# Kernel tuning notes

Measured on AMD Instinct MI355X. Metric: run time of the kernel, lower is better.

Reference implementation:

```python
import jax, jax.numpy as jnp
import numpy as np

NUM_HEADS = 12
HEAD_DIM = 64
EPS = 1e-6


def rms_norm(x, w):
    # normalize over last dim (head_dim)
    norm = jax.lax.rsqrt(jnp.mean(x * x, axis=-1, keepdims=True) + EPS)
    return x * norm * w


def apply_rotary_emb(x, cos, sin):
    x1, x2 = jnp.split(x, 2, axis=-1)
    return jnp.concatenate([x1 * cos - x2 * sin, x2 * cos + x1 * sin], axis=-1)


def setup_inputs() -> dict:
    key = jax.random.key(0)
    ks = jax.random.split(key, 6)
    B, N, C = 4, 2048, 768
    return {
        "x": jax.random.normal(ks[0], (B, N, C), dtype=jnp.float32),
        "cos": jax.random.uniform(ks[1], (1, 1, N, HEAD_DIM // 2), dtype=jnp.float32),
        "sin": jax.random.uniform(ks[2], (1, 1, N, HEAD_DIM // 2), dtype=jnp.float32),
        "qkv_w": jax.random.normal(ks[3], (3 * C, C), dtype=jnp.float32) * (C ** -0.5),
        "q_norm_w": jnp.ones((HEAD_DIM,), dtype=jnp.float32),
        "k_norm_w": jnp.ones((HEAD_DIM,), dtype=jnp.float32),
        "proj_w": jax.random.normal(ks[4], (C, C), dtype=jnp.float32) * (C ** -0.5),
        "proj_b": jnp.zeros((C,), dtype=jnp.float32),
    }


def reference(x, cos, sin, qkv_w, q_norm_w, k_norm_w, proj_w, proj_b):
    B, N, C = x.shape
    H, D = NUM_HEADS, HEAD_DIM
    scale = D ** -0.5
    # qkv projection: [B,N,3C] -> [3,B,H,N,D]
    qkv = jnp.einsum('bnc,oc->bno', x, qkv_w)
    qkv = qkv.reshape(B, N, 3, H, D).transpose(2, 0, 3, 1, 4)
    q, k, v = qkv[0], qkv[1], qkv[2]
    q = rms_norm(q, q_norm_w)
    k = rms_norm(k, k_norm_w)
    q = apply_rotary_emb(q, cos, sin)
    k = apply_rotary_emb(k, cos, sin)
    attn = jnp.einsum('bhqd,bhkd->bhqk', q, k) * scale
    attn = jax.nn.softmax(attn, axis=-1)
    out = jnp.einsum('bhqk,bhkd->bhqd', attn, v)
    out = out.transpose(0, 2, 1, 3).reshape(B, N, C)
    out = jnp.einsum('bnc,oc->bno', out, proj_w) + proj_b
    return out
```

## Files before the change

### kernel.cpp

```cpp
#include <hip/hip_runtime.h>
#include <hip/hip_bf16.h>

#define BB 4
#define NN 2048
#define CC 768
#define HH 12
#define DD 64

typedef __bf16 bf16;
typedef __attribute__((ext_vector_type(8))) __bf16 bf16x8;
typedef __attribute__((ext_vector_type(4))) __bf16 bf16x4;
typedef __attribute__((ext_vector_type(4))) float f32x4;

#define SZ_X    (BB * NN * CC)
#define SZ_QKVW (3 * CC * CC)
#define SZ_PW   (CC * CC)
#define SZ_QKV  ((size_t)BB * NN * 3 * CC)

#define OFF_X    0
#define OFF_QW   (OFF_X + SZ_X)
#define OFF_PW   (OFF_QW + SZ_QKVW)
#define OFF_QKV  (OFF_PW + SZ_PW)

__device__ __forceinline__ void async16(const bf16* g, bf16* l) {
    __builtin_amdgcn_global_load_lds(
        (const __attribute__((address_space(1))) unsigned int*)g,
        (__attribute__((address_space(3))) unsigned int*)l, 16, 0, 0);
}

__device__ __forceinline__ void cast8(const float* __restrict__ src,
                                      bf16* __restrict__ dst, int i) {
    f32x4 a = ((const f32x4*)src)[2 * i];
    f32x4 b = ((const f32x4*)src)[2 * i + 1];
    bf16x8 o;
#pragma unroll
    for (int j = 0; j < 4; ++j) { o[j] = (bf16)a[j]; o[j + 4] = (bf16)b[j]; }
    ((bf16x8*)dst)[i] = o;
}

__global__ __launch_bounds__(256) void convert3(
    const float* __restrict__ x, const float* __restrict__ qkvw,
    const float* __restrict__ pw, bf16* __restrict__ ws) {
    const int t = blockIdx.x * 256 + threadIdx.x;
    const int S = gridDim.x * 256;
    for (int i = t; i < SZ_X / 8;    i += S) cast8(x,    ws + OFF_X,  i);
    for (int i = t; i < SZ_QKVW / 8; i += S) cast8(qkvw, ws + OFF_QW, i);
    for (int i = t; i < SZ_PW / 8;   i += S) cast8(pw,   ws + OFF_PW, i);
}

__global__ __launch_bounds__(256) void gemm_qkv(
    const bf16* __restrict__ A, const bf16* __restrict__ W,
    bf16* __restrict__ C, bf16* __restrict__ Vt,
    const float* __restrict__ cosb, const float* __restrict__ sinb,
    const float* __restrict__ qw, const float* __restrict__ kw) {
    __shared__ __align__(16) bf16 As[128 * 64];
    __shared__ __align__(16) bf16 Bs[128 * 64];
    const int tid  = threadIdx.x;
    const int wave = tid >> 6;
    const int lane = tid & 63;
    const int quad = lane >> 4;
    const int l16  = lane & 15;
    const int m0 = blockIdx.y * 128;
    const int n0 = blockIdx.x * 128;
    const int wm = (wave >> 1) * 64;
    const int wn = (wave & 1) * 64;
    const int srow = lane >> 3;
    const int swz  = (lane & 7) ^ srow;
    const int K = CC;
    const int Nn = 3 * CC;

    f32x4 acc[4][4];
#pragma unroll
    for (int i = 0; i < 4; ++i)
#pragma unroll
        for (int j = 0; j < 4; ++j) acc[i][j] = (f32x4){0.f, 0.f, 0.f, 0.f};

    for (int k0 = 0; k0 < K; k0 += 64) {
#pragma unroll
        for (int i = 0; i < 4; ++i) {
            int row = i * 32 + wave * 8 + srow;
            async16(A + (size_t)(m0 + row) * CC + k0 + swz * 8,
                    &As[(i * 32 + wave * 8) * 64]);
            async16(W + (size_t)(n0 + row) * K + k0 + swz * 8,
                    &Bs[(i * 32 + wave * 8) * 64]);
        }
        __syncthreads();
#pragma unroll
        for (int kk = 0; kk < 2; ++kk) {
            const int slot = ((kk * 4 + quad) ^ (l16 & 7)) * 8;
            bf16x8 af[4], bf[4];
#pragma unroll
            for (int mt = 0; mt < 4; ++mt)
                af[mt] = *(const bf16x8*)(&As[(wm + mt * 16 + l16) * 64 + slot]);
#pragma unroll
            for (int nt = 0; nt < 4; ++nt)
                bf[nt] = *(const bf16x8*)(&Bs[(wn + nt * 16 + l16) * 64 + slot]);
#pragma unroll
            for (int mt = 0; mt < 4; ++mt)
#pragma unroll
                for (int nt = 0; nt < 4; ++nt)
                    acc[mt][nt] = __builtin_amdgcn_mfma_f32_16x16x32_bf16(
                        af[mt], bf[nt], acc[mt][nt], 0, 0, 0);
        }
        __syncthreads();
    }

    const int colblk = n0 + wn;
    const int sector = colblk / CC;
    if (sector == 2) {
        const int head = (colblk >> 6) - 24;
        const int btok = m0 + wm;
        const int bh   = (btok >> 11) * HH + head;
        const int nloc = btok & (NN - 1);
#pragma unroll
        for (int nt = 0; nt < 4; ++nt) {
            const int d = nt * 16 + l16;
            bf16* dst = Vt + ((size_t)bh * DD + d) * NN + nloc + quad * 4;
#pragma unroll
            for (int mt = 0; mt < 4; ++mt) {
                bf16x4 pk;
#pragma unroll
                for (int r = 0; r < 4; ++r) pk[r] = (bf16)acc[mt][nt][r];
                *(bf16x4*)(dst + mt * 16) = pk;
            }
        }
    } else {
        const float* wp = (sector == 0) ? qw : kw;
        const float qs = (sector == 0) ? 0.18033688f : 1.0f;
        float wv[4];
#pragma unroll
        for (int nt = 0; nt < 4; ++nt) wv[nt] = wp[nt * 16 + l16];
#pragma unroll
        for (int mt = 0; mt < 4; ++mt)
#pragma unroll
            for (int r = 0; r < 4; ++r) {
                const int row = m0 + wm + mt * 16 + quad * 4 + r;
                const int n   = row & (NN - 1);
                float v[4];
#pragma unroll
                for (int nt = 0; nt < 4; ++nt) v[nt] = acc[mt][nt][r];
                float ss = v[0] * v[0] + v[1] * v[1] + v[2] * v[2] + v[3] * v[3];
                ss += __shfl_xor(ss, 1, 64);
                ss += __shfl_xor(ss, 2, 64);
                ss += __shfl_xor(ss, 4, 64);
                ss += __shfl_xor(ss, 8, 64);
                const float rn = rsqrtf(ss * (1.0f / 64.0f) + 1e-6f);
#pragma unroll
                for (int nt = 0; nt < 4; ++nt) v[nt] *= rn * wv[nt];
                const float c0 = cosb[n * 32 + l16];
                const float c1 = cosb[n * 32 + 16 + l16];
                const float s0 = sinb[n * 32 + l16];
                const float s1 = sinb[n * 32 + 16 + l16];
                float y[4];
                y[0] = v[0] * c0 - v[2] * s0;
                y[1] = v[1] * c1 - v[3] * s1;
                y[2] = v[2] * c0 + v[0] * s0;
                y[3] = v[3] * c1 + v[1] * s1;
#pragma unroll
                for (int nt = 0; nt < 4; ++nt) {
                    int col = colblk + nt * 16 + l16;
                    C[(size_t)row * Nn + col] = (bf16)(y[nt] * qs);
                }
            }
    }
}

__global__ __launch_bounds__(256) void gemm_proj(
    const bf16* __restrict__ A, const bf16* __restrict__ W,
    const float* __restrict__ bias, float* __restrict__ C) {
    __shared__ __align__(16) bf16 As[128 * 64];
    __shared__ __align__(16) bf16 Bs[64 * 64];
    const int tid  = threadIdx.x;
    const int wave = tid >> 6;
    const int lane = tid & 63;
    const int quad = lane >> 4;
    const int l16  = lane & 15;
    const int m0 = blockIdx.y * 128;
    const int n0 = blockIdx.x * 64;
    const int wm = (wave >> 1) * 64;
    const int wn = (wave & 1) * 32;
    const int srow = lane >> 3;
    const int swz  = (lane & 7) ^ srow;
    const int lda = 3 * CC;
    const int K = CC;

    f32x4 acc[4][2];
#pragma unroll
    for (int i = 0; i < 4; ++i)
#pragma unroll
        for (int j = 0; j < 2; ++j) acc[i][j] = (f32x4){0.f, 0.f, 0.f, 0.f};

    for (int k0 = 0; k0 < K; k0 += 64) {
#pragma unroll
        for (int i = 0; i < 4; ++i) {
            int row = i * 32 + wave * 8 + srow;
            async16(A + (size_t)(m0 + row) * lda + k0 + swz * 8,
                    &As[(i * 32 + wave * 8) * 64]);
        }
#pragma unroll
        for (int i = 0; i < 2; ++i) {
            int row = i * 32 + wave * 8 + srow;
            async16(W + (size_t)(n0 + row) * K + k0 + swz * 8,
                    &Bs[(i * 32 + wave * 8) * 64]);
        }
        __syncthreads();
#pragma unroll
        for (int kk = 0; kk < 2; ++kk) {
            const int slot = ((kk * 4 + quad) ^ (l16 & 7)) * 8;
            bf16x8 af[4], bf[2];
#pragma unroll
            for (int mt = 0; mt < 4; ++mt)
                af[mt] = *(const bf16x8*)(&As[(wm + mt * 16 + l16) * 64 + slot]);
#pragma unroll
            for (int nt = 0; nt < 2; ++nt)
                bf[nt] = *(const bf16x8*)(&Bs[(wn + nt * 16 + l16) * 64 + slot]);
#pragma unroll
            for (int mt = 0; mt < 4; ++mt)
#pragma unroll
                for (int nt = 0; nt < 2; ++nt)
                    acc[mt][nt] = __builtin_amdgcn_mfma_f32_16x16x32_bf16(
                        af[mt], bf[nt], acc[mt][nt], 0, 0, 0);
        }
        __syncthreads();
    }
#pragma unroll
    for (int mt = 0; mt < 4; ++mt)
#pragma unroll
        for (int nt = 0; nt < 2; ++nt)
#pragma unroll
            for (int r = 0; r < 4; ++r) {
                int row = m0 + wm + mt * 16 + quad * 4 + r;
                int col = n0 + wn + nt * 16 + l16;
                C[(size_t)row * CC + col] = acc[mt][nt][r] + bias[col];
            }
}

__global__ __launch_bounds__(256) void flash_attn(
    const bf16* __restrict__ qkv, const bf16* __restrict__ Vt,
    bf16* __restrict__ Oqkv) {
    __shared__ __align__(16) bf16 Ks[64 * 64];
    __shared__ __align__(16) bf16 Vs[64 * 64];
    __shared__ __align__(16) bf16 Ps[4][32 * 72];
    const int tid  = threadIdx.x;
    const int wave = tid >> 6;
    const int lane = tid & 63;
    const int quad = lane >> 4;
    const int l16  = lane & 15;
    const int r7   = l16 & 7;
    const int bh = blockIdx.x;
    const int qt = blockIdx.y;
    const int b = bh / HH, h = bh % HH;
    const size_t rs = 3 * CC;
    const bf16* Qb  = qkv + (size_t)b * NN * rs + h * DD;
    const bf16* Kb  = Qb + CC;
    const bf16* Vtb = Vt + (size_t)bh * DD * NN;

    bf16x8 qf[2][2];
#pragma unroll
    for (int f = 0; f < 2; ++f) {
        const int qrow = qt * 128 + wave * 32 + f * 16 + l16;
#pragma unroll
        for (int hf = 0; hf < 2; ++hf)
            qf[f][hf] = *(const bf16x8*)(Qb + (size_t)qrow * rs + hf * 32 + quad * 8);
    }

    f32x4 accO[2][4];
#pragma unroll
    for (int f = 0; f < 2; ++f)
#pragma unroll
        for (int i = 0; i < 4; ++i) accO[f][i] = (f32x4){0.f, 0.f, 0.f, 0.f};
    float lsum[2] = {0.f, 0.f};

    const int srow = lane >> 3;
    const int swz  = (lane & 7) ^ srow;

    for (int kt = 0; kt < NN / 64; ++kt) {
#pragma unroll
        for (int i = 0; i < 2; ++i) {
            int row = i * 32 + wave * 8 + srow;
            async16(Kb + (size_t)(kt * 64 + row) * rs + swz * 8,
                    &Ks[(i * 32 + wave * 8) * 64]);
            async16(Vtb + (size_t)row * NN + kt * 64 + swz * 8,
                    &Vs[(i * 32 + wave * 8) * 64]);
        }
        __syncthreads();

        f32x4 s[2][4];
#pragma unroll
        for (int nt = 0; nt < 4; ++nt) {
            const int row = nt * 16 + l16;
            bf16x8 kf0 = *(const bf16x8*)(&Ks[row * 64 + (quad ^ r7) * 8]);
            bf16x8 kf1 = *(const bf16x8*)(&Ks[row * 64 + ((quad + 4) ^ r7) * 8]);
#pragma unroll
            for (int f = 0; f < 2; ++f) {
                f32x4 z = (f32x4){0.f, 0.f, 0.f, 0.f};
                z = __builtin_amdgcn_mfma_f32_16x16x32_bf16(kf0, qf[f][0], z, 0, 0, 0);
                s[f][nt] = __builtin_amdgcn_mfma_f32_16x16x32_bf16(kf1, qf[f][1], z, 0, 0, 0);
            }
        }

#pragma unroll
        for (int f = 0; f < 2; ++f)
#pragma unroll
            for (int nt = 0; nt < 4; ++nt) {
                bf16x4 pk;
#pragma unroll
                for (int r = 0; r < 4; ++r) {
                    float pv = __builtin_amdgcn_exp2f(s[f][nt][r]);
                    lsum[f] += pv;
                    pk[r] = (bf16)pv;
                }
                *(bf16x4*)(&Ps[wave][(f * 16 + l16) * 72 + nt * 16 + quad * 4]) = pk;
            }
        __asm__ volatile("s_waitcnt lgkmcnt(0)" ::: "memory");

        bf16x8 pf0[2], pf1[2];
#pragma unroll
        for (int f = 0; f < 2; ++f) {
            pf0[f] = *(const bf16x8*)(&Ps[wave][(f * 16 + l16) * 72 + quad * 8]);
            pf1[f] = *(const bf16x8*)(&Ps[wave][(f * 16 + l16) * 72 + 32 + quad * 8]);
        }
#pragma unroll
        for (int nt = 0; nt < 4; ++nt) {
            const int rowd = nt * 16 + l16;
            bf16x8 vf0 = *(const bf16x8*)(&Vs[rowd * 64 + (quad ^ r7) * 8]);
            bf16x8 vf1 = *(const bf16x8*)(&Vs[rowd * 64 + ((quad + 4) ^ r7) * 8]);
#pragma unroll
            for (int f = 0; f < 2; ++f) {
                accO[f][nt] = __builtin_amdgcn_mfma_f32_16x16x32_bf16(pf0[f], vf0, accO[f][nt], 0, 0, 0);
                accO[f][nt] = __builtin_amdgcn_mfma_f32_16x16x32_bf16(pf1[f], vf1, accO[f][nt], 0, 0, 0);
            }
        }
        __syncthreads();
    }

#pragma unroll
    for (int f = 0; f < 2; ++f) {
        lsum[f] += __shfl_xor(lsum[f], 16, 64);
        lsum[f] += __shfl_xor(lsum[f], 32, 64);
    }

#pragma unroll
    for (int f = 0; f < 2; ++f)
#pragma unroll
        for (int r = 0; r < 4; ++r) {
            float inv = 1.0f / __shfl(lsum[f], quad * 4 + r, 64);
            int n = qt * 128 + wave * 32 + f * 16 + quad * 4 + r;
#pragma unroll
            for (int nt = 0; nt < 4; ++nt) {
                int col = h * DD + nt * 16 + l16;
                Oqkv[(size_t)(b * NN + n) * rs + 2 * CC + col] = (bf16)(accO[f][nt][r] * inv);
            }
        }
}

extern "C" void kernel_launch(void* const* d_in, const int* in_sizes, int n_in,
                              void* d_out, int out_size, void* d_ws, size_t ws_size,
                              hipStream_t stream) {
    const float* x     = (const float*)d_in[0];
    const float* cosb  = (const float*)d_in[1];
    const float* sinb  = (const float*)d_in[2];
    const float* qkv_w = (const float*)d_in[3];
    const float* qnw   = (const float*)d_in[4];
    const float* knw   = (const float*)d_in[5];
    const float* pw    = (const float*)d_in[6];
    const float* pb    = (const float*)d_in[7];
    float* out = (float*)d_out;

    bf16* ws  = (bf16*)d_ws;
    bf16* xb  = ws + OFF_X;
    bf16* qwb = ws + OFF_QW;
    bf16* pwb = ws + OFF_PW;
    bf16* qkv = ws + OFF_QKV;
    bf16* vt  = (bf16*)d_out;

    const int M = BB * NN;

    convert3<<<1024, 256, 0, stream>>>(x, qkv_w, pw, ws);

    dim3 g1(3 * CC / 128, M / 128);
    gemm_qkv<<<g1, 256, 0, stream>>>(xb, qwb, qkv, vt, cosb, sinb, qnw, knw);

    dim3 g4(BB * HH, NN / 128);
    flash_attn<<<g4, 256, 0, stream>>>(qkv, vt, qkv);

    dim3 g5(CC / 64, M / 128);
    gemm_proj<<<g5, 256, 0, stream>>>(qkv + 2 * CC, pwb, pb, out);
}
```

Measured before the change: 231.4 us.

## Split flash attention work across 8 waves with 16 query rows each

The attention kernel now launches 512 threads per block, and each of 8 waves handles 16 query rows instead of 4 waves handling 32. K/V tile loads are spread over more threads, with one async load per thread per tile, and per-wave registers and P scratch shrink. This aims to raise parallelism and latency hiding. The cost is that each K/V fragment read from LDS is reused by only one query fragment, which doubles LDS reads per MFMA, and the block barriers now span more waves.

```diff
diff --git a/kernel.cpp b/kernel.cpp
--- a/kernel.cpp
+++ b/kernel.cpp
@@ -235,12 +235,12 @@
             }
 }
 
-__global__ __launch_bounds__(256) void flash_attn(
+__global__ __launch_bounds__(512) void flash_attn(
     const bf16* __restrict__ qkv, const bf16* __restrict__ Vt,
     bf16* __restrict__ Oqkv) {
     __shared__ __align__(16) bf16 Ks[64 * 64];
     __shared__ __align__(16) bf16 Vs[64 * 64];
-    __shared__ __align__(16) bf16 Ps[4][32 * 72];
+    __shared__ __align__(16) bf16 Ps[8][16 * 72];
     const int tid  = threadIdx.x;
     const int wave = tid >> 6;
     const int lane = tid & 63;
@@ -255,103 +255,80 @@
     const bf16* Kb  = Qb + CC;
     const bf16* Vtb = Vt + (size_t)bh * DD * NN;
 
-    bf16x8 qf[2][2];
-#pragma unroll
-    for (int f = 0; f < 2; ++f) {
-        const int qrow = qt * 128 + wave * 32 + f * 16 + l16;
+    bf16x8 qf[2];
+    {
+        const int qrow = qt * 128 + wave * 16 + l16;
 #pragma unroll
         for (int hf = 0; hf < 2; ++hf)
-            qf[f][hf] = *(const bf16x8*)(Qb + (size_t)qrow * rs + hf * 32 + quad * 8);
-    }
-
-    f32x4 accO[2][4];
-#pragma unroll
-    for (int f = 0; f < 2; ++f)
-#pragma unroll
-        for (int i = 0; i < 4; ++i) accO[f][i] = (f32x4){0.f, 0.f, 0.f, 0.f};
-    float lsum[2] = {0.f, 0.f};
+            qf[hf] = *(const bf16x8*)(Qb + (size_t)qrow * rs + hf * 32 + quad * 8);
+    }
+
+    f32x4 accO[4];
+#pragma unroll
+    for (int i = 0; i < 4; ++i) accO[i] = (f32x4){0.f, 0.f, 0.f, 0.f};
+    float lsum = 0.f;
 
     const int srow = lane >> 3;
     const int swz  = (lane & 7) ^ srow;
+    const int strow = wave * 8 + srow;
 
     for (int kt = 0; kt < NN / 64; ++kt) {
-#pragma unroll
-        for (int i = 0; i < 2; ++i) {
-            int row = i * 32 + wave * 8 + srow;
-            async16(Kb + (size_t)(kt * 64 + row) * rs + swz * 8,
-                    &Ks[(i * 32 + wave * 8) * 64]);
-            async16(Vtb + (size_t)row * NN + kt * 64 + swz * 8,
-                    &Vs[(i * 32 + wave * 8) * 64]);
-        }
-        __syncthreads();
-
-        f32x4 s[2][4];
+        async16(Kb + (size_t)(kt * 64 + strow) * rs + swz * 8,
+                &Ks[(wave * 8) * 64]);
+        async16(Vtb + (size_t)strow * NN + kt * 64 + swz * 8,
+                &Vs[(wave * 8) * 64]);
+        __syncthreads();
+
+        f32x4 s[4];
 #pragma unroll
         for (int nt = 0; nt < 4; ++nt) {
             const int row = nt * 16 + l16;
             bf16x8 kf0 = *(const bf16x8*)(&Ks[row * 64 + (quad ^ r7) * 8]);
             bf16x8 kf1 = *(const bf16x8*)(&Ks[row * 64 + ((quad + 4) ^ r7) * 8]);
-#pragma unroll
-            for (int f = 0; f < 2; ++f) {
-                f32x4 z = (f32x4){0.f, 0.f, 0.f, 0.f};
-                z = __builtin_amdgcn_mfma_f32_16x16x32_bf16(kf0, qf[f][0], z, 0, 0, 0);
-                s[f][nt] = __builtin_amdgcn_mfma_f32_16x16x32_bf16(kf1, qf[f][1], z, 0, 0, 0);
+            f32x4 z = (f32x4){0.f, 0.f, 0.f, 0.f};
+            z = __builtin_amdgcn_mfma_f32_16x16x32_bf16(kf0, qf[0], z, 0, 0, 0);
+            s[nt] = __builtin_amdgcn_mfma_f32_16x16x32_bf16(kf1, qf[1], z, 0, 0, 0);
+        }
+
+#pragma unroll
+        for (int nt = 0; nt < 4; ++nt) {
+            bf16x4 pk;
+#pragma unroll
+            for (int r = 0; r < 4; ++r) {
+                float pv = __builtin_amdgcn_exp2f(s[nt][r]);
+                lsum += pv;
+                pk[r] = (bf16)pv;
             }
-        }
-
-#pragma unroll
-        for (int f = 0; f < 2; ++f)
-#pragma unroll
-            for (int nt = 0; nt < 4; ++nt) {
-                bf16x4 pk;
-#pragma unroll
-                for (int r = 0; r < 4; ++r) {
-                    float pv = __builtin_amdgcn_exp2f(s[f][nt][r]);
-                    lsum[f] += pv;
-                    pk[r] = (bf16)pv;
-                }
-                *(bf16x4*)(&Ps[wave][(f * 16 + l16) * 72 + nt * 16 + quad * 4]) = pk;
-            }
+            *(bf16x4*)(&Ps[wave][l16 * 72 + nt * 16 + quad * 4]) = pk;
+        }
         __asm__ volatile("s_waitcnt lgkmcnt(0)" ::: "memory");
 
-        bf16x8 pf0[2], pf1[2];
-#pragma unroll
-        for (int f = 0; f < 2; ++f) {
-            pf0[f] = *(const bf16x8*)(&Ps[wave][(f * 16 + l16) * 72 + quad * 8]);
-            pf1[f] = *(const bf16x8*)(&Ps[wave][(f * 16 + l16) * 72 + 32 + quad * 8]);
-        }
+        bf16x8 pf0 = *(const bf16x8*)(&Ps[wave][l16 * 72 + quad * 8]);
+        bf16x8 pf1 = *(const bf16x8*)(&Ps[wave][l16 * 72 + 32 + quad * 8]);
 #pragma unroll
         for (int nt = 0; nt < 4; ++nt) {
             const int rowd = nt * 16 + l16;
             bf16x8 vf0 = *(const bf16x8*)(&Vs[rowd * 64 + (quad ^ r7) * 8]);
             bf16x8 vf1 = *(const bf16x8*)(&Vs[rowd * 64 + ((quad + 4) ^ r7) * 8]);
-#pragma unroll
-            for (int f = 0; f < 2; ++f) {
-                accO[f][nt] = __builtin_amdgcn_mfma_f32_16x16x32_bf16(pf0[f], vf0, accO[f][nt], 0, 0, 0);
-                accO[f][nt] = __builtin_amdgcn_mfma_f32_16x16x32_bf16(pf1[f], vf1, accO[f][nt], 0, 0, 0);
-            }
-        }
-        __syncthreads();
-    }
-
-#pragma unroll
-    for (int f = 0; f < 2; ++f) {
-        lsum[f] += __shfl_xor(lsum[f], 16, 64);
-        lsum[f] += __shfl_xor(lsum[f], 32, 64);
-    }
-
-#pragma unroll
-    for (int f = 0; f < 2; ++f)
-#pragma unroll
-        for (int r = 0; r < 4; ++r) {
-            float inv = 1.0f / __shfl(lsum[f], quad * 4 + r, 64);
-            int n = qt * 128 + wave * 32 + f * 16 + quad * 4 + r;
-#pragma unroll
-            for (int nt = 0; nt < 4; ++nt) {
-                int col = h * DD + nt * 16 + l16;
-                Oqkv[(size_t)(b * NN + n) * rs + 2 * CC + col] = (bf16)(accO[f][nt][r] * inv);
-            }
-        }
+            accO[nt] = __builtin_amdgcn_mfma_f32_16x16x32_bf16(pf0, vf0, accO[nt], 0, 0, 0);
+            accO[nt] = __builtin_amdgcn_mfma_f32_16x16x32_bf16(pf1, vf1, accO[nt], 0, 0, 0);
+        }
+        __syncthreads();
+    }
+
+    lsum += __shfl_xor(lsum, 16, 64);
+    lsum += __shfl_xor(lsum, 32, 64);
+
+#pragma unroll
+    for (int r = 0; r < 4; ++r) {
+        float inv = 1.0f / __shfl(lsum, quad * 4 + r, 64);
+        int n = qt * 128 + wave * 16 + quad * 4 + r;
+#pragma unroll
+        for (int nt = 0; nt < 4; ++nt) {
+            int col = h * DD + nt * 16 + l16;
+            Oqkv[(size_t)(b * NN + n) * rs + 2 * CC + col] = (bf16)(accO[nt][r] * inv);
+        }
+    }
 }
 
 extern "C" void kernel_launch(void* const* d_in, const int* in_sizes, int n_in,
@@ -382,7 +359,7 @@
     gemm_qkv<<<g1, 256, 0, stream>>>(xb, qwb, qkv, vt, cosb, sinb, qnw, knw);
 
     dim3 g4(BB * HH, NN / 128);
-    flash_attn<<<g4, 256, 0, stream>>>(qkv, vt, qkv);
+    flash_attn<<<g4, 512, 0, stream>>>(qkv, vt, qkv);
 
     dim3 g5(CC / 64, M / 128);
     gemm_proj<<<g5, 256, 0, stream>>>(qkv + 2 * CC, pwb, pb, out);
```

After: 228.9 us. About the same (-1.1%).

## Split attention KV loop across two wave groups with shared-memory reduction

Applied to the files above, without the earlier changes.

The flash attention block grows from 4 to 8 waves. Each half processes alternating 64-key tiles for the same 128 query rows, so every iteration loads two K/V tiles at once. At the end the second group writes its partial output and row sums to shared memory, and the first group adds them before normalizing and storing. This targets low latency hiding and the limited parallelism of a 384-block grid. In exchange it adds LDS use, a final reduction with an extra barrier, and larger blocks that may lower occupancy.

```diff
diff --git a/kernel.cpp b/kernel.cpp
--- a/kernel.cpp
+++ b/kernel.cpp
@@ -235,14 +235,16 @@
             }
 }
 
-__global__ __launch_bounds__(256) void flash_attn(
+__global__ __launch_bounds__(512) void flash_attn(
     const bf16* __restrict__ qkv, const bf16* __restrict__ Vt,
     bf16* __restrict__ Oqkv) {
-    __shared__ __align__(16) bf16 Ks[64 * 64];
-    __shared__ __align__(16) bf16 Vs[64 * 64];
-    __shared__ __align__(16) bf16 Ps[4][32 * 72];
+    __shared__ __align__(16) bf16 Ks[2][64 * 64];
+    __shared__ __align__(16) bf16 Vs[2][64 * 64];
+    __shared__ __align__(16) bf16 Ps[8][32 * 72];
     const int tid  = threadIdx.x;
     const int wave = tid >> 6;
+    const int w4   = wave & 3;
+    const int half = wave >> 2;
     const int lane = tid & 63;
     const int quad = lane >> 4;
     const int l16  = lane & 15;
@@ -258,7 +260,7 @@
     bf16x8 qf[2][2];
 #pragma unroll
     for (int f = 0; f < 2; ++f) {
-        const int qrow = qt * 128 + wave * 32 + f * 16 + l16;
+        const int qrow = qt * 128 + w4 * 32 + f * 16 + l16;
 #pragma unroll
         for (int hf = 0; hf < 2; ++hf)
             qf[f][hf] = *(const bf16x8*)(Qb + (size_t)qrow * rs + hf * 32 + quad * 8);
@@ -271,26 +273,31 @@
         for (int i = 0; i < 4; ++i) accO[f][i] = (f32x4){0.f, 0.f, 0.f, 0.f};
     float lsum[2] = {0.f, 0.f};
 
-    const int srow = lane >> 3;
-    const int swz  = (lane & 7) ^ srow;
-
-    for (int kt = 0; kt < NN / 64; ++kt) {
-#pragma unroll
-        for (int i = 0; i < 2; ++i) {
-            int row = i * 32 + wave * 8 + srow;
-            async16(Kb + (size_t)(kt * 64 + row) * rs + swz * 8,
-                    &Ks[(i * 32 + wave * 8) * 64]);
-            async16(Vtb + (size_t)row * NN + kt * 64 + swz * 8,
-                    &Vs[(i * 32 + wave * 8) * 64]);
-        }
-        __syncthreads();
+    const int srow  = lane >> 3;
+    const int swz   = (lane & 7) ^ srow;
+    const int strow = wave * 8 + srow;
+
+    for (int step = 0; step < NN / 128; ++step) {
+        const int t0 = step * 2;
+        async16(Kb + (size_t)(t0 * 64 + strow) * rs + swz * 8,
+                &Ks[0][(wave * 8) * 64]);
+        async16(Kb + (size_t)((t0 + 1) * 64 + strow) * rs + swz * 8,
+                &Ks[1][(wave * 8) * 64]);
+        async16(Vtb + (size_t)strow * NN + t0 * 64 + swz * 8,
+                &Vs[0][(wave * 8) * 64]);
+        async16(Vtb + (size_t)strow * NN + (t0 + 1) * 64 + swz * 8,
+                &Vs[1][(wave * 8) * 64]);
+        __syncthreads();
+
+        const bf16* Kc = Ks[half];
+        const bf16* Vc = Vs[half];
 
         f32x4 s[2][4];
 #pragma unroll
         for (int nt = 0; nt < 4; ++nt) {
             const int row = nt * 16 + l16;
-            bf16x8 kf0 = *(const bf16x8*)(&Ks[row * 64 + (quad ^ r7) * 8]);
-            bf16x8 kf1 = *(const bf16x8*)(&Ks[row * 64 + ((quad + 4) ^ r7) * 8]);
+            bf16x8 kf0 = *(const bf16x8*)(&Kc[row * 64 + (quad ^ r7) * 8]);
+            bf16x8 kf1 = *(const bf16x8*)(&Kc[row * 64 + ((quad + 4) ^ r7) * 8]);
 #pragma unroll
             for (int f = 0; f < 2; ++f) {
                 f32x4 z = (f32x4){0.f, 0.f, 0.f, 0.f};
@@ -323,8 +330,8 @@
 #pragma unroll
         for (int nt = 0; nt < 4; ++nt) {
             const int rowd = nt * 16 + l16;
-            bf16x8 vf0 = *(const bf16x8*)(&Vs[rowd * 64 + (quad ^ r7) * 8]);
-            bf16x8 vf1 = *(const bf16x8*)(&Vs[rowd * 64 + ((quad + 4) ^ r7) * 8]);
+            bf16x8 vf0 = *(const bf16x8*)(&Vc[rowd * 64 + (quad ^ r7) * 8]);
+            bf16x8 vf1 = *(const bf16x8*)(&Vc[rowd * 64 + ((quad + 4) ^ r7) * 8]);
 #pragma unroll
             for (int f = 0; f < 2; ++f) {
                 accO[f][nt] = __builtin_amdgcn_mfma_f32_16x16x32_bf16(pf0[f], vf0, accO[f][nt], 0, 0, 0);
@@ -340,18 +347,46 @@
         lsum[f] += __shfl_xor(lsum[f], 32, 64);
     }
 
-#pragma unroll
-    for (int f = 0; f < 2; ++f)
-#pragma unroll
-        for (int r = 0; r < 4; ++r) {
-            float inv = 1.0f / __shfl(lsum[f], quad * 4 + r, 64);
-            int n = qt * 128 + wave * 32 + f * 16 + quad * 4 + r;
-#pragma unroll
-            for (int nt = 0; nt < 4; ++nt) {
-                int col = h * DD + nt * 16 + l16;
-                Oqkv[(size_t)(b * NN + n) * rs + 2 * CC + col] = (bf16)(accO[f][nt][r] * inv);
-            }
-        }
+    float* Osc = (float*)&Ps[0][0];
+    float* Ls  = Osc + 4 * 32 * 65;
+    if (wave >= 4) {
+#pragma unroll
+        for (int f = 0; f < 2; ++f) {
+            if (quad == 0) Ls[w4 * 32 + f * 16 + l16] = lsum[f];
+#pragma unroll
+            for (int nt = 0; nt < 4; ++nt)
+#pragma unroll
+                for (int r = 0; r < 4; ++r)
+                    Osc[(w4 * 32 + f * 16 + quad * 4 + r) * 65 + nt * 16 + l16] =
+                        accO[f][nt][r];
+        }
+    }
+    __syncthreads();
+    if (wave < 4) {
+#pragma unroll
+        for (int f = 0; f < 2; ++f) {
+            lsum[f] += Ls[w4 * 32 + f * 16 + l16];
+#pragma unroll
+            for (int nt = 0; nt < 4; ++nt)
+#pragma unroll
+                for (int r = 0; r < 4; ++r)
+                    accO[f][nt][r] +=
+                        Osc[(w4 * 32 + f * 16 + quad * 4 + r) * 65 + nt * 16 + l16];
+        }
+#pragma unroll
+        for (int f = 0; f < 2; ++f)
+#pragma unroll
+            for (int r = 0; r < 4; ++r) {
+                float inv = 1.0f / __shfl(lsum[f], quad * 4 + r, 64);
+                int n = qt * 128 + w4 * 32 + f * 16 + quad * 4 + r;
+#pragma unroll
+                for (int nt = 0; nt < 4; ++nt) {
+                    int col = h * DD + nt * 16 + l16;
+                    Oqkv[(size_t)(b * NN + n) * rs + 2 * CC + col] =
+                        (bf16)(accO[f][nt][r] * inv);
+                }
+            }
+    }
 }
 
 extern "C" void kernel_launch(void* const* d_in, const int* in_sizes, int n_in,
@@ -382,7 +417,7 @@
     gemm_qkv<<<g1, 256, 0, stream>>>(xb, qwb, qkv, vt, cosb, sinb, qnw, knw);
 
     dim3 g4(BB * HH, NN / 128);
-    flash_attn<<<g4, 256, 0, stream>>>(qkv, vt, qkv);
+    flash_attn<<<g4, 512, 0, stream>>>(qkv, vt, qkv);
 
     dim3 g5(CC / 64, M / 128);
     gemm_proj<<<g5, 256, 0, stream>>>(qkv + 2 * CC, pwb, pb, out);
```

Result: no change. 231.1 us (-0.2%).

## Double-buffer K/V tiles in flash attention with async prefetch two tiles ahead

Applied to the files above, without the earlier changes.

Splits the shared-memory K and V tiles into two buffers and issues the async loads for tile kt+2 while tile kt+1 is already resident. Explicit vmcnt waits and raw barriers replace the per-iteration __syncthreads, so global-load latency can overlap with the MFMA and softmax work. LDS use doubles from 16KB to 32KB for K/V, which may reduce occupancy. Correctness depends on the hand-counted vmcnt values matching the number of outstanding loads.

```diff
diff --git a/kernel.cpp b/kernel.cpp
--- a/kernel.cpp
+++ b/kernel.cpp
@@ -238,8 +238,8 @@
 __global__ __launch_bounds__(256) void flash_attn(
     const bf16* __restrict__ qkv, const bf16* __restrict__ Vt,
     bf16* __restrict__ Oqkv) {
-    __shared__ __align__(16) bf16 Ks[64 * 64];
-    __shared__ __align__(16) bf16 Vs[64 * 64];
+    __shared__ __align__(16) bf16 Ks[2][64 * 64];
+    __shared__ __align__(16) bf16 Vs[2][64 * 64];
     __shared__ __align__(16) bf16 Ps[4][32 * 72];
     const int tid  = threadIdx.x;
     const int wave = tid >> 6;
@@ -255,6 +255,9 @@
     const bf16* Kb  = Qb + CC;
     const bf16* Vtb = Vt + (size_t)bh * DD * NN;
 
+    const int srow = lane >> 3;
+    const int swz  = (lane & 7) ^ srow;
+
     bf16x8 qf[2][2];
 #pragma unroll
     for (int f = 0; f < 2; ++f) {
@@ -263,6 +266,18 @@
         for (int hf = 0; hf < 2; ++hf)
             qf[f][hf] = *(const bf16x8*)(Qb + (size_t)qrow * rs + hf * 32 + quad * 8);
     }
+    __asm__ volatile("s_waitcnt vmcnt(0)" ::: "memory");
+
+#define STAGE(bufi, t)                                                        \
+    do {                                                                      \
+        _Pragma("unroll") for (int i_ = 0; i_ < 2; ++i_) {                    \
+            int row_ = i_ * 32 + wave * 8 + srow;                             \
+            async16(Kb + (size_t)((t) * 64 + row_) * rs + swz * 8,            \
+                    &Ks[bufi][(i_ * 32 + wave * 8) * 64]);                    \
+            async16(Vtb + (size_t)row_ * NN + (t) * 64 + swz * 8,             \
+                    &Vs[bufi][(i_ * 32 + wave * 8) * 64]);                    \
+        }                                                                     \
+    } while (0)
 
     f32x4 accO[2][4];
 #pragma unroll
@@ -271,26 +286,23 @@
         for (int i = 0; i < 4; ++i) accO[f][i] = (f32x4){0.f, 0.f, 0.f, 0.f};
     float lsum[2] = {0.f, 0.f};
 
-    const int srow = lane >> 3;
-    const int swz  = (lane & 7) ^ srow;
-
-    for (int kt = 0; kt < NN / 64; ++kt) {
-#pragma unroll
-        for (int i = 0; i < 2; ++i) {
-            int row = i * 32 + wave * 8 + srow;
-            async16(Kb + (size_t)(kt * 64 + row) * rs + swz * 8,
-                    &Ks[(i * 32 + wave * 8) * 64]);
-            async16(Vtb + (size_t)row * NN + kt * 64 + swz * 8,
-                    &Vs[(i * 32 + wave * 8) * 64]);
-        }
-        __syncthreads();
+    STAGE(0, 0);
+    STAGE(1, 1);
+    __asm__ volatile("s_waitcnt vmcnt(4)" ::: "memory");
+    __builtin_amdgcn_s_barrier();
+
+    const int NT = NN / 64;
+    for (int kt = 0; kt < NT; ++kt) {
+        const int cur = kt & 1;
+        const bf16* Kc = Ks[cur];
+        const bf16* Vc = Vs[cur];
 
         f32x4 s[2][4];
 #pragma unroll
         for (int nt = 0; nt < 4; ++nt) {
             const int row = nt * 16 + l16;
-            bf16x8 kf0 = *(const bf16x8*)(&Ks[row * 64 + (quad ^ r7) * 8]);
-            bf16x8 kf1 = *(const bf16x8*)(&Ks[row * 64 + ((quad + 4) ^ r7) * 8]);
+            bf16x8 kf0 = *(const bf16x8*)(&Kc[row * 64 + (quad ^ r7) * 8]);
+            bf16x8 kf1 = *(const bf16x8*)(&Kc[row * 64 + ((quad + 4) ^ r7) * 8]);
 #pragma unroll
             for (int f = 0; f < 2; ++f) {
                 f32x4 z = (f32x4){0.f, 0.f, 0.f, 0.f};
@@ -323,16 +335,25 @@
 #pragma unroll
         for (int nt = 0; nt < 4; ++nt) {
             const int rowd = nt * 16 + l16;
-            bf16x8 vf0 = *(const bf16x8*)(&Vs[rowd * 64 + (quad ^ r7) * 8]);
-            bf16x8 vf1 = *(const bf16x8*)(&Vs[rowd * 64 + ((quad + 4) ^ r7) * 8]);
+            bf16x8 vf0 = *(const bf16x8*)(&Vc[rowd * 64 + (quad ^ r7) * 8]);
+            bf16x8 vf1 = *(const bf16x8*)(&Vc[rowd * 64 + ((quad + 4) ^ r7) * 8]);
 #pragma unroll
             for (int f = 0; f < 2; ++f) {
                 accO[f][nt] = __builtin_amdgcn_mfma_f32_16x16x32_bf16(pf0[f], vf0, accO[f][nt], 0, 0, 0);
                 accO[f][nt] = __builtin_amdgcn_mfma_f32_16x16x32_bf16(pf1[f], vf1, accO[f][nt], 0, 0, 0);
             }
         }
-        __syncthreads();
-    }
+
+        __builtin_amdgcn_s_barrier();
+        if (kt + 2 < NT) {
+            STAGE(cur, kt + 2);
+            __asm__ volatile("s_waitcnt vmcnt(4)" ::: "memory");
+        } else if (kt + 1 < NT) {
+            __asm__ volatile("s_waitcnt vmcnt(0)" ::: "memory");
+        }
+        __builtin_amdgcn_s_barrier();
+    }
+#undef STAGE
 
 #pragma unroll
     for (int f = 0; f < 2; ++f) {
```

Result: slower. 249.2 us (+7.7%).
